# Kernel optimization log

Measured on AMD Instinct MI355X. Metric: run time of the kernel, lower is better.

Reference implementation:

```python
import jax, jax.numpy as jnp
import numpy as np

KERNEL = 11  # matches AttnBlock(kernel_size=11)
EPS = 1e-4


def _patches(x, k):
    """Extract k x k patches (stride 1, VALID), matching nn.Unfold ordering.

    x: [B, C, H, W] -> ([B, L, C*k*k], (Hp, Wp)) with L = Hp*Wp.
    """
    p = jax.lax.conv_general_dilated_patches(x, (k, k), (1, 1), 'VALID')  # [B, C*k*k, Hp, Wp]
    B, D, Hp, Wp = p.shape
    return p.reshape(B, D, Hp * Wp).transpose(0, 2, 1), (Hp, Wp)


def setup_inputs() -> dict:
    key = jax.random.key(0)
    k1, k2 = jax.random.split(key)
    im1 = jax.random.normal(k1, (4, 64, 40, 40), dtype=jnp.float32)
    im2 = jax.random.normal(k2, (4, 64, 40, 40), dtype=jnp.float32)
    return {"im1": im1, "im2": im2}


def reference(im1, im2):
    k = KERNEL
    # Dynamic per-sample filters from im1 patches, L2-normalized per patch.
    p1, _ = _patches(im1, k)                                  # [B, L, D], D = C*k*k
    norm = jnp.sqrt(jnp.sum(p1 * p1, axis=-1, keepdims=True))  # [B, L, 1]
    p1n = p1 / jnp.maximum(norm, EPS)
    # conv2d(im2, filters) with stride 1 / no padding == dot of im2 patches with filters.
    p2, (Hp, Wp) = _patches(im2, k)                           # [B, P, D], P = Hp*Wp
    scores = jnp.einsum('bld,bpd->bpl', p1n, p2)              # [B, P, L]
    out = jnp.max(scores, axis=-1)                            # max over filter (channel) dim
    B = im1.shape[0]
    return out.reshape(B, 1, Hp, Wp)
```

## Files before the change

kernel.cpp:

```cpp
#include <hip/hip_runtime.h>

#define C_    64
#define H_    40
#define W_    40
#define KS    11
#define HP    30
#define NB    4
#define NL    900
#define ND    59
#define EPSF  1e-4f
#define PCH   6
#define PCHB  10
#define NCHB  3
#define NPLMAX (PCHB + KS - 1)
#define SCW   65
#define NINF  -3.4e38f
#define MPAD  1664
#define GBLK  1600
#define GBATCH (1600 * 1600)
#define GSTEPT 65600

typedef _Float16 f16x8 __attribute__((ext_vector_type(8)));
typedef float    f32x4 __attribute__((ext_vector_type(4)));

__global__ __launch_bounds__(128)
void k_pack(const float* __restrict__ im2, const float* __restrict__ im1,
            _Float16* __restrict__ packed, float* __restrict__ ssqbuf,
            unsigned int* __restrict__ keys) {
    const int blk = blockIdx.x, b = blockIdx.y, img = blockIdx.z;
    const int pos = blk * 128 + threadIdx.x;
    const float* src = (img ? im1 : im2) + b * C_ * 1600;
    _Float16* dst = packed + ((size_t)img * NB + b) * (8 * MPAD * 8);
    float ss = 0.f;
    #pragma unroll
    for (int oct = 0; oct < 8; ++oct) {
        f16x8 h = {};
        if (pos < 1600) {
            #pragma unroll
            for (int j = 0; j < 8; ++j) {
                float v = src[(oct * 8 + j) * 1600 + pos];
                h[j] = (_Float16)v;
                ss += v * v;
            }
        }
        *(f16x8*)&dst[(oct * MPAD + pos) * 8] = h;
    }
    if (img == 1 && pos < 1600) ssqbuf[b * 1600 + pos] = ss;
    if (img == 0 && pos < NL) keys[b * NL + pos] = 0u;
}

__global__ __launch_bounds__(256, 3)
void k_gram(const _Float16* __restrict__ packed, _Float16* __restrict__ G,
            const float* __restrict__ ssqbuf, float* __restrict__ invnorm) {
    const int i = blockIdx.x, j = blockIdx.y, b = blockIdx.z;
    const int tid = threadIdx.x;
    __shared__ __align__(16) _Float16 smem[128 * 136];

    int dd = i - j; if (dd < 0) dd = -dd;
    if (dd > 10) {
        if (i < j) {
            const int part = (j == 11) ? 0 : ((i == 0) ? 1 : 2);
            const int ly0 = part * 10;
            float* ssq = (float*)smem;
            float* colsum = ssq + 800;
            for (int t = tid; t < 800; t += 256)
                ssq[t] = ssqbuf[b * 1600 + ly0 * W_ + t];
            __syncthreads();
            for (int t = tid; t < 10 * W_; t += 256) {
                int yy = t / W_, x = t - yy * W_;
                float s = 0.f;
                #pragma unroll
                for (int r = 0; r < KS; ++r) s += ssq[(yy + r) * W_ + x];
                colsum[t] = s;
            }
            __syncthreads();
            for (int t = tid; t < 10 * HP; t += 256) {
                int ly = t / HP, lx = t - ly * HP;
                float s = 0.f;
                #pragma unroll
                for (int sx = 0; sx < KS; ++sx) s += colsum[ly * W_ + lx + sx];
                invnorm[b * NL + (ly0 + ly) * HP + lx] = 1.f / fmaxf(sqrtf(s), EPSF);
            }
        }
        return;
    }
    const int w = tid >> 6, L = tid & 63, lq = L >> 4, lr = L & 15;

    _Float16 (*As)[128][8] = (_Float16 (*)[128][8])smem;
    _Float16 (*Bs)[128][8] = (_Float16 (*)[128][8])(smem + 8192);

    const _Float16* pa = packed + (size_t)b * (8 * MPAD * 8);
    const _Float16* pb = packed + (size_t)(NB + b) * (8 * MPAD * 8);
    for (int t = tid; t < 1024; t += 256) {
        int oct = t >> 7, m = t & 127;
        *(f16x8*)&As[oct][m][0] = *(const f16x8*)&pa[(oct * MPAD + i * 128 + m) * 8];
        *(f16x8*)&Bs[oct][m][0] = *(const f16x8*)&pb[(oct * MPAD + j * 128 + m) * 8];
    }
    __syncthreads();

    const int mb = (w & 1) * 64, nb = (w >> 1) * 64;
    f16x8 a0[4], a1[4], b0[4], b1[4];
    #pragma unroll
    for (int q = 0; q < 4; ++q) {
        a0[q] = *(const f16x8*)&As[lq][mb + q * 16 + lr][0];
        a1[q] = *(const f16x8*)&As[4 + lq][mb + q * 16 + lr][0];
        b0[q] = *(const f16x8*)&Bs[lq][nb + q * 16 + lr][0];
        b1[q] = *(const f16x8*)&Bs[4 + lq][nb + q * 16 + lr][0];
    }
    f32x4 acc[4][4];
    #pragma unroll
    for (int mi = 0; mi < 4; ++mi)
        #pragma unroll
        for (int ni = 0; ni < 4; ++ni) {
            f32x4 c = {0.f, 0.f, 0.f, 0.f};
            c = __builtin_amdgcn_mfma_f32_16x16x32_f16(a0[mi], b0[ni], c, 0, 0, 0);
            c = __builtin_amdgcn_mfma_f32_16x16x32_f16(a1[mi], b1[ni], c, 0, 0, 0);
            acc[mi][ni] = c;
        }
    __syncthreads();
    #pragma unroll
    for (int mi = 0; mi < 4; ++mi)
        #pragma unroll
        for (int ni = 0; ni < 4; ++ni)
            #pragma unroll
            for (int rg = 0; rg < 4; ++rg)
                smem[(mb + mi * 16 + lq * 4 + rg) * 136 + nb + ni * 16 + lr] =
                    (_Float16)acc[mi][ni][rg];
    __syncthreads();
    _Float16* Gb = G + (size_t)b * GBATCH;
    for (int t = tid; t < 2048; t += 256) {
        int row = t >> 4, seg = t & 15;
        int m = i * 128 + row, n = j * 128 + seg * 8;
        if (m < 1600 && n < 1600) {
            int r = m / 40, mr = m - r * 40;
            int c = n / 40, nc = n - c * 40;
            *(f16x8*)&Gb[(size_t)(r * 40 + c) * GBLK + mr * 40 + nc] =
                *(const f16x8*)&smem[row * 136 + seg * 8];
        }
    }
}

__global__ __launch_bounds__(256, 2)
void k_box(const _Float16* __restrict__ G, const float* __restrict__ invnorm,
           unsigned int* __restrict__ keys) {
    __shared__ __align__(16) _Float16 pl_lds[NPLMAX * GBLK];
    __shared__ float csum2[2 * 1600];
    __shared__ float sInv[PCHB * HP];
    const int chunk = blockIdx.x;
    const int dy = (int)blockIdx.y - (HP - 1);
    const int b = blockIdx.z;
    const int ady = dy < 0 ? -dy : dy;
    const int rows = HP - ady;
    if (chunk * PCHB >= rows) return;
    const int pyLo = dy < 0 ? -dy : 0;
    const int py0 = pyLo + chunk * PCHB;
    const int P = min(PCHB, rows - chunk * PCHB);
    const int nPl = P + KS - 1;
    const int tid = threadIdx.x;

    const _Float16* Gb = G + (size_t)b * GBATCH + (size_t)(py0 * 41 + dy) * GBLK;
    for (int t = tid; t < nPl * 200; t += 256) {
        int pl = t / 200, e = t - pl * 200;
        *(f16x8*)&pl_lds[pl * GBLK + e * 8] = *(const f16x8*)&Gb[pl * GSTEPT + e * 8];
    }
    for (int t = tid; t < P * HP; t += 256) {
        int i = t / HP, lx = t - i * HP;
        sInv[i * HP + lx] = invnorm[b * NL + (py0 + i + dy) * HP + lx];
    }
    __syncthreads();

    float s[8];
    if (tid < 200) {
        #pragma unroll
        for (int j = 0; j < 8; ++j) s[j] = 0.f;
        for (int r = 0; r < KS; ++r) {
            f16x8 q = *(const f16x8*)&pl_lds[r * GBLK + tid * 8];
            #pragma unroll
            for (int j = 0; j < 8; ++j) s[j] += (float)q[j];
        }
    }

    for (int i = 0; i < P; ++i) {
        float* cb = csum2 + (i & 1) * 1600;
        if (tid < 200) {
            if (i > 0) {
                f16x8 qa = *(const f16x8*)&pl_lds[(i + 10) * GBLK + tid * 8];
                f16x8 qs = *(const f16x8*)&pl_lds[(i - 1) * GBLK + tid * 8];
                #pragma unroll
                for (int j = 0; j < 8; ++j) s[j] += (float)qa[j] - (float)qs[j];
            }
            float4* c4 = (float4*)(cb + tid * 8);
            c4[0] = make_float4(s[0], s[1], s[2], s[3]);
            c4[1] = make_float4(s[4], s[5], s[6], s[7]);
        }
        __syncthreads();
        if (tid < 240) {
            int px = tid >> 3, l = tid & 7;
            const float* cp = cb + px * 40;
            const float* inv = sInv + i * HP;
            float m = NINF;
            #pragma unroll
            for (int k = 0; k < 4; ++k) {
                int lx = l + 8 * k;
                if (lx < HP) {
                    const float* cpl = cp + lx;
                    float run = 0.f;
                    #pragma unroll
                    for (int sr = 0; sr < KS; ++sr) run += cpl[sr * 41];
                    m = fmaxf(m, run * inv[lx]);
                }
            }
            m = fmaxf(m, __shfl_xor(m, 1));
            m = fmaxf(m, __shfl_xor(m, 2));
            m = fmaxf(m, __shfl_xor(m, 4));
            if (l == 0) {
                unsigned int ub = __float_as_uint(m);
                unsigned int k2 = (ub & 0x80000000u) ? ~ub : (ub | 0x80000000u);
                atomicMax(&keys[b * NL + (py0 + i) * HP + px], k2);
            }
        }
    }
}

__global__ __launch_bounds__(256)
void k_decode(const unsigned int* __restrict__ keys, float* __restrict__ out) {
    int i = blockIdx.x * 256 + threadIdx.x;
    if (i < NB * NL) {
        unsigned int k = keys[i];
        unsigned int u = (k & 0x80000000u) ? (k ^ 0x80000000u) : ~k;
        out[i] = __uint_as_float(u);
    }
}

__global__ __launch_bounds__(256)
void k_norm_fb(const float* __restrict__ im1, float* __restrict__ invnorm) {
    const int ly = blockIdx.x, b = blockIdx.y;
    const int tid = threadIdx.x;
    __shared__ float colsq[KS * W_];
    __shared__ float colsum[W_];
    const float* base = im1 + b * C_ * H_ * W_;
    for (int i = tid; i < KS * W_; i += 256) {
        int r = i / W_, x = i - r * W_;
        const float* p = base + (ly + r) * W_ + x;
        float s = 0.f;
        #pragma unroll 8
        for (int c = 0; c < C_; ++c) { float v = p[c * H_ * W_]; s += v * v; }
        colsq[i] = s;
    }
    __syncthreads();
    if (tid < W_) {
        float s = 0.f;
        #pragma unroll
        for (int r = 0; r < KS; ++r) s += colsq[r * W_ + tid];
        colsum[tid] = s;
    }
    __syncthreads();
    if (tid < HP) {
        float s = 0.f;
        #pragma unroll
        for (int sx = 0; sx < KS; ++sx) s += colsum[tid + sx];
        invnorm[b * NL + ly * HP + tid] = 1.f / fmaxf(sqrtf(s), EPSF);
    }
}

#define MAXPL 16
__global__ __launch_bounds__(256, 2)
void k_main_fb(const float* __restrict__ im1, const float* __restrict__ im2,
               const float* __restrict__ invnorm, unsigned int* __restrict__ keys) {
    const int chunk = blockIdx.x;
    const int dy = (int)blockIdx.y - (HP - 1);
    const int b = blockIdx.z;
    const int ady = dy < 0 ? -dy : dy;
    const int rows = HP - ady;
    if (chunk * PCH >= rows) return;
    const int pyLo = dy < 0 ? -dy : 0;
    const int py0 = pyLo + chunk * PCH;
    const int P = min(PCH, rows - chunk * PCH);
    const int nPl = P + KS - 1;
    const int tid = threadIdx.x;
    const int w = tid >> 6, L = tid & 63, lq = L >> 4, lr = L & 15;

    __shared__ __align__(16) _Float16 planes[MAXPL][H_ * W_];
    __shared__ __align__(16) float csum[H_ * W_];
    __shared__ __align__(16) _Float16 Astg[8][48][8];
    __shared__ __align__(16) _Float16 Bstg[8][48][8];
    __shared__ float scratch[HP * SCW];
    __shared__ float partials[120];
    __shared__ float sInv[HP];

    const float* im1b = im1 + b * C_ * H_ * W_;
    const float* im2b = im2 + b * C_ * H_ * W_;
    if (tid < 128) {
        int arr = tid >> 6, r = tid & 63;
        int oct = r >> 3, x = 40 + (r & 7);
        f16x8 z = {};
        *(f16x8*)((arr ? Bstg : Astg)[oct][x]) = z;
    }
    for (int p = 0; p < nPl; ++p) {
        const int y = py0 + p;
        for (int t = tid; t < 640; t += 256) {
            int arr = t >= 320;
            int r = arr ? t - 320 : t;
            int oct = r / 40, x = r - oct * 40;
            const float* pc = (arr ? (im1b + (y + dy) * W_) : (im2b + y * W_))
                              + oct * 8 * H_ * W_ + x;
            f16x8 h;
            #pragma unroll
            for (int j = 0; j < 8; ++j) h[j] = (_Float16)pc[j * H_ * W_];
            *(f16x8*)((arr ? Bstg : Astg)[oct][x]) = h;
        }
        __syncthreads();
        for (int t = w; t < 9; t += 4) {
            int mt = t / 3, nt = t - 3 * mt;
            f16x8 a0 = *(const f16x8*)(Astg[lq][mt * 16 + lr]);
            f16x8 b0 = *(const f16x8*)(Bstg[lq][nt * 16 + lr]);
            f16x8 a1 = *(const f16x8*)(Astg[4 + lq][mt * 16 + lr]);
            f16x8 b1 = *(const f16x8*)(Bstg[4 + lq][nt * 16 + lr]);
            f32x4 acc = {0.f, 0.f, 0.f, 0.f};
            acc = __builtin_amdgcn_mfma_f32_16x16x32_f16(a0, b0, acc, 0, 0, 0);
            acc = __builtin_amdgcn_mfma_f32_16x16x32_f16(a1, b1, acc, 0, 0, 0);
            int x1 = nt * 16 + lr;
            if (x1 < W_) {
                int x2b = mt * 16 + lq * 4;
                #pragma unroll
                for (int rg = 0; rg < 4; ++rg) {
                    int x2 = x2b + rg;
                    if (x2 < W_) planes[p][x2 * W_ + x1] = (_Float16)acc[rg];
                }
            }
        }
        __syncthreads();
    }
    for (int i = 0; i < P; ++i) {
        const int py = py0 + i, ly = py + dy;
        if (tid < 200) {
            float4* c4 = (float4*)(csum + tid * 8);
            if (i == 0) {
                float s[8] = {0.f,0.f,0.f,0.f,0.f,0.f,0.f,0.f};
                #pragma unroll
                for (int r = 0; r < KS; ++r) {
                    f16x8 q = *(const f16x8*)(planes[r] + tid * 8);
                    #pragma unroll
                    for (int j = 0; j < 8; ++j) s[j] += (float)q[j];
                }
                c4[0] = make_float4(s[0], s[1], s[2], s[3]);
                c4[1] = make_float4(s[4], s[5], s[6], s[7]);
            } else {
                f16x8 qa = *(const f16x8*)(planes[i + 10] + tid * 8);
                f16x8 qs = *(const f16x8*)(planes[i - 1] + tid * 8);
                float4 v0 = c4[0], v1 = c4[1];
                v0.x += (float)qa[0] - (float)qs[0]; v0.y += (float)qa[1] - (float)qs[1];
                v0.z += (float)qa[2] - (float)qs[2]; v0.w += (float)qa[3] - (float)qs[3];
                v1.x += (float)qa[4] - (float)qs[4]; v1.y += (float)qa[5] - (float)qs[5];
                v1.z += (float)qa[6] - (float)qs[6]; v1.w += (float)qa[7] - (float)qs[7];
                c4[0] = v0; c4[1] = v1;
            }
        } else if (tid >= 224 && tid < 224 + HP) {
            sInv[tid - 224] = invnorm[b * NL + ly * HP + (tid - 224)];
        }
        __syncthreads();
        for (int t = tid; t < 5 * ND; t += 256) {
            int pg = t / ND, dxI = t - ND * pg;
            int dx = dxI - (HP - 1), pxb = 6 * pg;
            #pragma unroll
            for (int u = 0; u < 6; ++u) scratch[(pxb + u) * SCW + dxI] = NINF;
            int u0 = max(0, -dx - pxb), u1 = min(5, (HP - 1) - dx - pxb);
            if (u0 <= u1) {
                const float* cp = csum + dx;
                float run = 0.f;
                #pragma unroll
                for (int sr = 0; sr < KS; ++sr) run += cp[(pxb + u0 + sr) * (W_ + 1)];
                int u = u0;
                for (;;) {
                    scratch[(pxb + u) * SCW + dxI] = run * sInv[pxb + u + dx];
                    if (++u > u1) break;
                    run += cp[(pxb + u + 10) * (W_ + 1)] - cp[(pxb + u - 1) * (W_ + 1)];
                }
            }
        }
        __syncthreads();
        if (tid < 120) {
            int px = tid >> 2, q = tid & 3;
            float m = NINF;
            int d0 = q * 15, d1 = min(d0 + 15, ND);
            for (int d = d0; d < d1; ++d) m = fmaxf(m, scratch[px * SCW + d]);
            partials[tid] = m;
        }
        __syncthreads();
        if (tid < HP) {
            float m = fmaxf(fmaxf(partials[tid * 4], partials[tid * 4 + 1]),
                            fmaxf(partials[tid * 4 + 2], partials[tid * 4 + 3]));
            unsigned int ub = __float_as_uint(m);
            unsigned int k = (ub & 0x80000000u) ? ~ub : (ub | 0x80000000u);
            atomicMax(&keys[b * NL + py * HP + tid], k);
        }
        __syncthreads();
    }
}

extern "C" void kernel_launch(void* const* d_in, const int* in_sizes, int n_in,
                              void* d_out, int out_size, void* d_ws, size_t ws_size,
                              hipStream_t stream) {
    const float* im1 = (const float*)d_in[0];
    const float* im2 = (const float*)d_in[1];
    unsigned int* keys = (unsigned int*)d_ws;
    float* invnorm = (float*)((char*)d_ws + 14400);
    float* ssqbuf  = (float*)((char*)d_ws + 28800);
    const size_t packedOff = 65536;
    const size_t packedBytes = (size_t)2 * NB * 8 * MPAD * 8 * 2;
    const size_t gOff = packedOff + packedBytes;
    const size_t gBytes = (size_t)NB * GBATCH * 2;
    const size_t needed = gOff + gBytes;

    if (ws_size >= needed) {
        _Float16* packed = (_Float16*)((char*)d_ws + packedOff);
        _Float16* G = (_Float16*)((char*)d_ws + gOff);
        k_pack<<<dim3(13, NB, 2), 128, 0, stream>>>(im2, im1, packed, ssqbuf, keys);
        k_gram<<<dim3(13, 13, NB), 256, 0, stream>>>(packed, G, ssqbuf, invnorm);
        k_box<<<dim3(NCHB, ND, NB), 256, 0, stream>>>(G, invnorm, keys);
    } else {
        hipMemsetAsync(d_ws, 0, NB * NL * sizeof(unsigned int), stream);
        k_norm_fb<<<dim3(HP, NB), 256, 0, stream>>>(im1, invnorm);
        k_main_fb<<<dim3(5, ND, NB), 256, 0, stream>>>(im1, im2, invnorm, keys);
    }
    k_decode<<<(NB * NL + 255) / 256, 256, 0, stream>>>(keys, (float*)d_out);
}
```

Measured before the change: 92.52 us.

## Fuse Gram computation and norm into box kernel, drop global G buffer

Removes the separate k_gram kernel and its global fp16 Gram matrix. Each box block now computes the Gram-row slices it needs with MFMA straight into LDS, and derives the inverse norms from the squared-sum buffer locally. This avoids writing and re-reading a large G array and drops one launch, but overlapping blocks recompute the same Gram tiles many times, and operands are loaded from global memory without LDS staging.

```diff
diff --git a/kernel.cpp b/kernel.cpp
--- a/kernel.cpp
+++ b/kernel.cpp
@@ -17,8 +17,6 @@
 #define NINF  -3.4e38f
 #define MPAD  1664
 #define GBLK  1600
-#define GBATCH (1600 * 1600)
-#define GSTEPT 65600
 
 typedef _Float16 f16x8 __attribute__((ext_vector_type(8)));
 typedef float    f32x4 __attribute__((ext_vector_type(4)));
@@ -49,100 +47,9 @@
     if (img == 0 && pos < NL) keys[b * NL + pos] = 0u;
 }
 
-__global__ __launch_bounds__(256, 3)
-void k_gram(const _Float16* __restrict__ packed, _Float16* __restrict__ G,
-            const float* __restrict__ ssqbuf, float* __restrict__ invnorm) {
-    const int i = blockIdx.x, j = blockIdx.y, b = blockIdx.z;
-    const int tid = threadIdx.x;
-    __shared__ __align__(16) _Float16 smem[128 * 136];
-
-    int dd = i - j; if (dd < 0) dd = -dd;
-    if (dd > 10) {
-        if (i < j) {
-            const int part = (j == 11) ? 0 : ((i == 0) ? 1 : 2);
-            const int ly0 = part * 10;
-            float* ssq = (float*)smem;
-            float* colsum = ssq + 800;
-            for (int t = tid; t < 800; t += 256)
-                ssq[t] = ssqbuf[b * 1600 + ly0 * W_ + t];
-            __syncthreads();
-            for (int t = tid; t < 10 * W_; t += 256) {
-                int yy = t / W_, x = t - yy * W_;
-                float s = 0.f;
-                #pragma unroll
-                for (int r = 0; r < KS; ++r) s += ssq[(yy + r) * W_ + x];
-                colsum[t] = s;
-            }
-            __syncthreads();
-            for (int t = tid; t < 10 * HP; t += 256) {
-                int ly = t / HP, lx = t - ly * HP;
-                float s = 0.f;
-                #pragma unroll
-                for (int sx = 0; sx < KS; ++sx) s += colsum[ly * W_ + lx + sx];
-                invnorm[b * NL + (ly0 + ly) * HP + lx] = 1.f / fmaxf(sqrtf(s), EPSF);
-            }
-        }
-        return;
-    }
-    const int w = tid >> 6, L = tid & 63, lq = L >> 4, lr = L & 15;
-
-    _Float16 (*As)[128][8] = (_Float16 (*)[128][8])smem;
-    _Float16 (*Bs)[128][8] = (_Float16 (*)[128][8])(smem + 8192);
-
-    const _Float16* pa = packed + (size_t)b * (8 * MPAD * 8);
-    const _Float16* pb = packed + (size_t)(NB + b) * (8 * MPAD * 8);
-    for (int t = tid; t < 1024; t += 256) {
-        int oct = t >> 7, m = t & 127;
-        *(f16x8*)&As[oct][m][0] = *(const f16x8*)&pa[(oct * MPAD + i * 128 + m) * 8];
-        *(f16x8*)&Bs[oct][m][0] = *(const f16x8*)&pb[(oct * MPAD + j * 128 + m) * 8];
-    }
-    __syncthreads();
-
-    const int mb = (w & 1) * 64, nb = (w >> 1) * 64;
-    f16x8 a0[4], a1[4], b0[4], b1[4];
-    #pragma unroll
-    for (int q = 0; q < 4; ++q) {
-        a0[q] = *(const f16x8*)&As[lq][mb + q * 16 + lr][0];
-        a1[q] = *(const f16x8*)&As[4 + lq][mb + q * 16 + lr][0];
-        b0[q] = *(const f16x8*)&Bs[lq][nb + q * 16 + lr][0];
-        b1[q] = *(const f16x8*)&Bs[4 + lq][nb + q * 16 + lr][0];
-    }
-    f32x4 acc[4][4];
-    #pragma unroll
-    for (int mi = 0; mi < 4; ++mi)
-        #pragma unroll
-        for (int ni = 0; ni < 4; ++ni) {
-            f32x4 c = {0.f, 0.f, 0.f, 0.f};
-            c = __builtin_amdgcn_mfma_f32_16x16x32_f16(a0[mi], b0[ni], c, 0, 0, 0);
-            c = __builtin_amdgcn_mfma_f32_16x16x32_f16(a1[mi], b1[ni], c, 0, 0, 0);
-            acc[mi][ni] = c;
-        }
-    __syncthreads();
-    #pragma unroll
-    for (int mi = 0; mi < 4; ++mi)
-        #pragma unroll
-        for (int ni = 0; ni < 4; ++ni)
-            #pragma unroll
-            for (int rg = 0; rg < 4; ++rg)
-                smem[(mb + mi * 16 + lq * 4 + rg) * 136 + nb + ni * 16 + lr] =
-                    (_Float16)acc[mi][ni][rg];
-    __syncthreads();
-    _Float16* Gb = G + (size_t)b * GBATCH;
-    for (int t = tid; t < 2048; t += 256) {
-        int row = t >> 4, seg = t & 15;
-        int m = i * 128 + row, n = j * 128 + seg * 8;
-        if (m < 1600 && n < 1600) {
-            int r = m / 40, mr = m - r * 40;
-            int c = n / 40, nc = n - c * 40;
-            *(f16x8*)&Gb[(size_t)(r * 40 + c) * GBLK + mr * 40 + nc] =
-                *(const f16x8*)&smem[row * 136 + seg * 8];
-        }
-    }
-}
-
 __global__ __launch_bounds__(256, 2)
-void k_box(const _Float16* __restrict__ G, const float* __restrict__ invnorm,
-           unsigned int* __restrict__ keys) {
+void k_boxf(const _Float16* __restrict__ packed, const float* __restrict__ ssqbuf,
+            unsigned int* __restrict__ keys) {
     __shared__ __align__(16) _Float16 pl_lds[NPLMAX * GBLK];
     __shared__ float csum2[2 * 1600];
     __shared__ float sInv[PCHB * HP];
@@ -157,15 +64,55 @@
     const int P = min(PCHB, rows - chunk * PCHB);
     const int nPl = P + KS - 1;
     const int tid = threadIdx.x;
-
-    const _Float16* Gb = G + (size_t)b * GBATCH + (size_t)(py0 * 41 + dy) * GBLK;
-    for (int t = tid; t < nPl * 200; t += 256) {
-        int pl = t / 200, e = t - pl * 200;
-        *(f16x8*)&pl_lds[pl * GBLK + e * 8] = *(const f16x8*)&Gb[pl * GSTEPT + e * 8];
-    }
+    const int w = tid >> 6, L = tid & 63, lq = L >> 4, lr = L & 15;
+
+    const int ly0 = py0 + dy;
+    float* ssqS = csum2;
+    float* colV = csum2 + 800;
+    for (int t = tid; t < nPl * 40; t += 256)
+        ssqS[t] = ssqbuf[b * 1600 + ly0 * 40 + t];
+
+    const _Float16* pa = packed + (size_t)b * (8 * MPAD * 8);
+    const _Float16* pb = packed + (size_t)(NB + b) * (8 * MPAD * 8);
+    for (int p = 0; p < nPl; ++p) {
+        const int posA = (py0 + p) * 40;
+        const int posB = (py0 + p + dy) * 40;
+        for (int t = w; t < 9; t += 4) {
+            int mt = t / 3, nt = t - 3 * mt;
+            f16x8 a0 = *(const f16x8*)&pa[((size_t)lq * MPAD + posA + mt * 16 + lr) * 8];
+            f16x8 a1 = *(const f16x8*)&pa[((size_t)(4 + lq) * MPAD + posA + mt * 16 + lr) * 8];
+            f16x8 b0 = *(const f16x8*)&pb[((size_t)lq * MPAD + posB + nt * 16 + lr) * 8];
+            f16x8 b1 = *(const f16x8*)&pb[((size_t)(4 + lq) * MPAD + posB + nt * 16 + lr) * 8];
+            f32x4 acc = {0.f, 0.f, 0.f, 0.f};
+            acc = __builtin_amdgcn_mfma_f32_16x16x32_f16(a0, b0, acc, 0, 0, 0);
+            acc = __builtin_amdgcn_mfma_f32_16x16x32_f16(a1, b1, acc, 0, 0, 0);
+            int x1 = nt * 16 + lr;
+            if (x1 < 40) {
+                int x2b = mt * 16 + lq * 4;
+                #pragma unroll
+                for (int rg = 0; rg < 4; ++rg) {
+                    int x2 = x2b + rg;
+                    if (x2 < 40) pl_lds[p * GBLK + x2 * 40 + x1] = (_Float16)acc[rg];
+                }
+            }
+        }
+    }
+    __syncthreads();
+
+    for (int t = tid; t < P * 40; t += 256) {
+        int i = t / 40, x = t - i * 40;
+        float s2 = 0.f;
+        #pragma unroll
+        for (int r = 0; r < KS; ++r) s2 += ssqS[(i + r) * 40 + x];
+        colV[t] = s2;
+    }
+    __syncthreads();
     for (int t = tid; t < P * HP; t += 256) {
         int i = t / HP, lx = t - i * HP;
-        sInv[i * HP + lx] = invnorm[b * NL + (py0 + i + dy) * HP + lx];
+        float s2 = 0.f;
+        #pragma unroll
+        for (int sx = 0; sx < KS; ++sx) s2 += colV[i * 40 + lx + sx];
+        sInv[t] = 1.f / fmaxf(sqrtf(s2), EPSF);
     }
     __syncthreads();
 
@@ -408,16 +355,12 @@
     float* ssqbuf  = (float*)((char*)d_ws + 28800);
     const size_t packedOff = 65536;
     const size_t packedBytes = (size_t)2 * NB * 8 * MPAD * 8 * 2;
-    const size_t gOff = packedOff + packedBytes;
-    const size_t gBytes = (size_t)NB * GBATCH * 2;
-    const size_t needed = gOff + gBytes;
+    const size_t needed = packedOff + packedBytes;
 
     if (ws_size >= needed) {
         _Float16* packed = (_Float16*)((char*)d_ws + packedOff);
-        _Float16* G = (_Float16*)((char*)d_ws + gOff);
         k_pack<<<dim3(13, NB, 2), 128, 0, stream>>>(im2, im1, packed, ssqbuf, keys);
-        k_gram<<<dim3(13, 13, NB), 256, 0, stream>>>(packed, G, ssqbuf, invnorm);
-        k_box<<<dim3(NCHB, ND, NB), 256, 0, stream>>>(G, invnorm, keys);
+        k_boxf<<<dim3(NCHB, ND, NB), 256, 0, stream>>>(packed, ssqbuf, keys);
     } else {
         hipMemsetAsync(d_ws, 0, NB * NL * sizeof(unsigned int), stream);
         k_norm_fb<<<dim3(HP, NB), 256, 0, stream>>>(im1, invnorm);
```

New measurement: 105.6 us. +14.1%, slower.
